# Kernel optimization log

Hardware: AMD Instinct MI355X
Metric: run time of the kernel (lower is better)

The kernel has to match this reference:

```python
import jax, jax.numpy as jnp
import numpy as np

B = 64            # graphs in batch
N = 100_000       # total nodes
E = 600_000       # total edges of g == nodes of line graph lg
E2 = 1_500_000    # edges of line graph
H = 128           # hidden_dim
L = 3             # num_layers
MAXZ = 100

seg_sum = jax.ops.segment_sum


def setup_inputs() -> dict:
    key = jax.random.key(0)
    ks = jax.random.split(key, 20)
    s = 1.0 / np.sqrt(H)
    inp = {
        'z': jax.random.randint(ks[0], (N,), 0, MAXZ + 1),
        'd': jax.random.uniform(ks[1], (E, 1), dtype=jnp.float32),
        'src': jax.random.randint(ks[2], (E,), 0, N),
        'dst': jax.random.randint(ks[3], (E,), 0, N),
        'lsrc': jax.random.randint(ks[4], (E2,), 0, E),
        'ldst': jax.random.randint(ks[5], (E2,), 0, E),
        'node_graph': jnp.sort(jax.random.randint(ks[6], (N,), 0, B)),
        'edge_graph': jnp.sort(jax.random.randint(ks[7], (E,), 0, B)),
        'emb': jax.random.normal(ks[8], (MAXZ + 1, H), jnp.float32),
        'ep_w': jax.random.normal(ks[9], (1, H), jnp.float32) * s,
        'ep_b': jnp.zeros((H,), jnp.float32),
        'gW': jax.random.normal(ks[10], (L, H, H), jnp.float32) * s,
        'gb': jnp.zeros((L, H), jnp.float32),
        'lgW': jax.random.normal(ks[11], (L, H, H), jnp.float32) * s,
        'lgb': jnp.zeros((L, H), jnp.float32),
        'r1w': jax.random.normal(ks[12], (2 * H, H), jnp.float32) * s,
        'r1b': jnp.zeros((H,), jnp.float32),
        'r2w': jax.random.normal(ks[13], (H, 1), jnp.float32) * s,
        'r2b': jnp.zeros((1,), jnp.float32),
    }
    return inp


def _graph_conv(h, srcix, dstix, W, b, n_nodes):
    # DGL GraphConv, norm='both', aggregate-then-weight (in==out dims):
    # h' = D_in^{-1/2} * A^T * (D_out^{-1/2} * h) @ W + b, degrees clamped >= 1
    ones = jnp.ones(srcix.shape[0], h.dtype)
    deg_out = jnp.clip(seg_sum(ones, srcix, num_segments=n_nodes), 1.0)
    deg_in = jnp.clip(seg_sum(ones, dstix, num_segments=n_nodes), 1.0)
    m = h * (deg_out ** -0.5)[:, None]
    agg = seg_sum(m[srcix], dstix, num_segments=n_nodes)  # SpMM gather-scatter
    agg = agg * (deg_in ** -0.5)[:, None]
    return agg @ W + b


def _segment_mean(h, seg, n_seg):
    sums = seg_sum(h, seg, num_segments=n_seg)
    cnt = jnp.clip(seg_sum(jnp.ones(h.shape[0], h.dtype), seg, num_segments=n_seg), 1.0)
    return sums / cnt[:, None]


def reference(z, d, src, dst, lsrc, ldst, node_graph, edge_graph,
              emb, ep_w, ep_b, gW, gb, lgW, lgb, r1w, r1b, r2w, r2b):
    h = emb[z]                       # [N, H]
    e = d @ ep_w + ep_b              # [E, H]
    for i in range(L):
        h = jax.nn.relu(_graph_conv(h, src, dst, gW[i], gb[i], N))
    for i in range(L):
        e = jax.nn.relu(_graph_conv(e, lsrc, ldst, lgW[i], lgb[i], E))
    hg = _segment_mean(h, node_graph, B)   # [B, H]
    he = _segment_mean(e, edge_graph, B)   # [B, H]
    x = jnp.concatenate([hg, he], axis=-1)  # [B, 2H]
    y = jax.nn.silu(x @ r1w + r1b) @ r2w + r2b
    return y.reshape(-1)             # [B]
```

## Files before the change

### kernel.cpp

```cpp
#include <hip/hip_runtime.h>
#include <math.h>

#define H 128
typedef unsigned short u16;
typedef unsigned char u8;
typedef unsigned int u32;
typedef _Float16 f16;
typedef f16 f16x8 __attribute__((ext_vector_type(8)));
typedef float f32x4 __attribute__((ext_vector_type(4)));
typedef float f32x2 __attribute__((ext_vector_type(2)));

#if __has_builtin(__builtin_amdgcn_cvt_pk_fp8_f32)
#define HW8 1
#else
#define HW8 0
#endif

#define SSTRIDE 144

static inline int cdiv(long long a, long long b) { return (int)((a + b - 1) / b); }

struct F8 {
    static __device__ inline float dec(u8 v) {
        int e = (v >> 3) & 15, m = v & 7;
        float f = (e == 0) ? (float)m * 0.001953125f : ldexpf(1.f + 0.125f * (float)m, e - 7);
        return (v & 0x80) ? -f : f;
    }
    static __device__ inline u8 enc(float x) {
        u8 s = (u8)((__float_as_uint(x) >> 24) & 0x80);
        float ax = fabsf(x);
        if (!(ax < 448.f)) return s | 0x7E;
        if (ax < 0.015625f) {
            int m = (int)rintf(ax * 512.f);
            if (m >= 8) return s | 0x08;
            return s | (u8)m;
        }
        int e; float fr = frexpf(ax, &e);
        int E = e - 1;
        int m = (int)rintf(fr * 16.f - 8.f);
        if (m == 8) { m = 0; ++E; }
        if (E > 8) return s | 0x7E;
        return s | (u8)(((E + 7) << 3) | m);
    }
};

static __device__ inline u32 enc4(float x0, float x1, float x2, float x3) {
#if HW8
    u32 w = __builtin_amdgcn_cvt_pk_fp8_f32(x0, x1, 0, false);
    w = __builtin_amdgcn_cvt_pk_fp8_f32(x2, x3, w, true);
    return w;
#else
    union { u8 b[4]; u32 u; } p;
    p.b[0] = F8::enc(x0); p.b[1] = F8::enc(x1); p.b[2] = F8::enc(x2); p.b[3] = F8::enc(x3);
    return p.u;
#endif
}
static __device__ inline float4 dec4(u32 v) {
#if HW8
    f32x2 lo = __builtin_amdgcn_cvt_pk_f32_fp8(v, false);
    f32x2 hi = __builtin_amdgcn_cvt_pk_f32_fp8(v, true);
    return make_float4(lo.x, lo.y, hi.x, hi.y);
#else
    union { u32 u; u8 b[4]; } c; c.u = v;
    return make_float4(F8::dec(c.b[0]), F8::dec(c.b[1]), F8::dec(c.b[2]), F8::dec(c.b[3]));
#endif
}
static __device__ inline float dec1(u8 b) {
#if HW8
    return __builtin_amdgcn_cvt_f32_fp8((int)b, 0);
#else
    return F8::dec(b);
#endif
}

__global__ __launch_bounds__(256) void setup1_k(
    const float* __restrict__ gW, const float* __restrict__ lgW, f16* __restrict__ wt, int L, int nbPW,
    const int* __restrict__ src, const int* __restrict__ dst,
    const int* __restrict__ lsrc, const int* __restrict__ ldst,
    int* __restrict__ con, int* __restrict__ cin, int* __restrict__ coe, int* __restrict__ cie,
    int E, int E2, int nbHI,
    const int* __restrict__ node_graph, int N, const int* __restrict__ edge_graph,
    int B, int* __restrict__ cntn, int* __restrict__ cnte) {
    int blk = blockIdx.x;
    if (blk < nbPW) {
        int mat = blk >> 6;
        int idx = (blk & 63) * 256 + threadIdx.x;
        int k = idx >> 7, n = idx & 127;
        const float* W = (mat < L) ? gW + (size_t)mat * H * H : lgW + (size_t)(mat - L) * H * H;
        wt[(size_t)mat * H * H + (size_t)n * H + k] = (f16)W[(size_t)k * H + n];
        return;
    }
    blk -= nbPW;
    if (blk < nbHI) {
        int i = blk * 256 + threadIdx.x;
        if (i < E) {
            atomicAdd(&con[src[i]], 1);
            atomicAdd(&cin[dst[i]], 1);
        } else if (i < E + E2) {
            int j = i - E;
            atomicAdd(&coe[lsrc[j]], 1);
            atomicAdd(&cie[ldst[j]], 1);
        }
        return;
    }
    blk -= nbHI;
    {
        const int* seg = blk ? edge_graph : node_graph;
        int n = blk ? E : N;
        int* cnt = blk ? cnte : cntn;
        __shared__ int bound[129];
        int b = threadIdx.x;
        if (b <= B) {
            int lo = 0, hi = n;
            while (lo < hi) {
                int mid = (lo + hi) >> 1;
                if (seg[mid] < b) lo = mid + 1; else hi = mid;
            }
            bound[b] = lo;
        }
        __syncthreads();
        if (b < B) cnt[b] = bound[b + 1] - bound[b];
    }
}

__global__ __launch_bounds__(256) void setup2_k(
    const int* __restrict__ con, const int* __restrict__ cin,
    const int* __restrict__ coe, const int* __restrict__ cie,
    float* __restrict__ ron, float* __restrict__ rin,
    float* __restrict__ roe, float* __restrict__ rie,
    const float* __restrict__ d, float2* __restrict__ pairE, int N, int E, int nbRS,
    int* __restrict__ offs_n, int nbN, int* __restrict__ offs_e, int* __restrict__ bsum) {
    int blk = blockIdx.x;
    if (blk < nbRS) {
        int i = blk * 256 + threadIdx.x;
        if (i < N) { int v = con[i]; ron[i] = rsqrtf((float)(v < 1 ? 1 : v)); }
        else if (i < 2 * N) { int n = i - N; int v = cin[n]; rin[n] = rsqrtf((float)(v < 1 ? 1 : v)); }
        else if (i < 2 * N + E) {
            int n = i - 2 * N; int v = coe[n];
            float r = rsqrtf((float)(v < 1 ? 1 : v));
            roe[n] = r;
            pairE[n] = make_float2(r * d[n], r);
        } else if (i < 2 * N + 2 * E) {
            int n = i - 2 * N - E; int v = cie[n]; rie[n] = rsqrtf((float)(v < 1 ? 1 : v));
        }
        return;
    }
    blk -= nbRS;
    {
        __shared__ int sh[256];
        const int* in; int* out; int n; int gid;
        if (blk < nbN) { in = cin; out = offs_n; n = N; gid = blk * 256 + threadIdx.x; }
        else { in = cie; out = offs_e; n = E; gid = (blk - nbN) * 256 + threadIdx.x; }
        int v = (gid < n) ? in[gid] : 0;
        sh[threadIdx.x] = v;
        __syncthreads();
        for (int off = 1; off < 256; off <<= 1) {
            int t = (threadIdx.x >= off) ? sh[threadIdx.x - off] : 0;
            __syncthreads();
            sh[threadIdx.x] += t;
            __syncthreads();
        }
        if (gid < n) out[gid] = sh[threadIdx.x] - v;
        if (threadIdx.x == 255) bsum[blk] = sh[255];
    }
}

__global__ __launch_bounds__(256) void scan_bsum2_k(int* __restrict__ bsum, int nbA, int nbB) {
    __shared__ int sh[256];
    __shared__ int carry;
#pragma unroll 1
    for (int part = 0; part < 2; ++part) {
        int base0 = part ? nbA : 0;
        int nb = part ? nbB : nbA;
        if (threadIdx.x == 0) carry = 0;
        __syncthreads();
        for (int base = 0; base < nb; base += 256) {
            int i = base + threadIdx.x;
            int v = (i < nb) ? bsum[base0 + i] : 0;
            sh[threadIdx.x] = v;
            __syncthreads();
            for (int off = 1; off < 256; off <<= 1) {
                int t = (threadIdx.x >= off) ? sh[threadIdx.x - off] : 0;
                __syncthreads();
                sh[threadIdx.x] += t;
                __syncthreads();
            }
            if (i < nb) bsum[base0 + i] = sh[threadIdx.x] - v + carry;
            __syncthreads();
            if (threadIdx.x == 0) carry += sh[255];
            __syncthreads();
        }
    }
}

__global__ __launch_bounds__(256) void setup3_k(
    int* __restrict__ offs_n, int* __restrict__ cur_n, int N, int nbN, int E,
    int* __restrict__ offs_e, int* __restrict__ cur_e, int E2, int nbE,
    const int* __restrict__ bsum,
    const int* __restrict__ z, const float* __restrict__ emb,
    const float* __restrict__ ron, u8* __restrict__ featN) {
    int blk = blockIdx.x;
    int nbSA = nbN + nbE;
    if (blk < nbSA) {
        int* offs; int* curp; int n; int gid; int nnz;
        if (blk < nbN) { offs = offs_n; curp = cur_n; n = N; gid = blk * 256 + threadIdx.x; nnz = E; }
        else { offs = offs_e; curp = cur_e; n = E; gid = (blk - nbN) * 256 + threadIdx.x; nnz = E2; }
        if (gid < n) {
            int v = offs[gid] + bsum[blk];
            offs[gid] = v;
            curp[gid] = v;
        }
        if (gid == 0) offs[n] = nnz;
        return;
    }
    blk -= nbSA;
    {
        int idx = blk * 256 + threadIdx.x;
        if (idx >= N * 32) return;
        int n = idx >> 5, c4 = (idx & 31) << 2;
        float sc = ron[n];
        const float4 v = *(const float4*)(emb + (size_t)z[n] * H + c4);
        *(u32*)(featN + (size_t)n * H + c4) = enc4(v.x * sc, v.y * sc, v.z * sc, v.w * sc);
    }
}

__global__ __launch_bounds__(256) void fill2_k(const int* __restrict__ src, const int* __restrict__ dst,
                                               const int* __restrict__ lsrc, const int* __restrict__ ldst,
                                               int* __restrict__ cur_n, int* __restrict__ cur_e,
                                               uint2* __restrict__ nbr_n, uint2* __restrict__ nbr_e,
                                               int E, int E2) {
    int i = blockIdx.x * 256 + threadIdx.x;
    if (i < E) {
        int dd = dst[i];
        int p = atomicAdd(&cur_n[dd], 1);
        nbr_n[p] = make_uint2((u32)src[i], (u32)dd);
    } else if (i < E + E2) {
        int j = i - E;
        int dd = ldst[j];
        int p = atomicAdd(&cur_e[dd], 1);
        nbr_e[p] = make_uint2((u32)lsrc[j], (u32)dd);
    }
}

template <bool STORE>
__device__ __forceinline__ void conv_mfma_phase(
    u8* __restrict__ Xout, const f16* __restrict__ Wt, const float* __restrict__ bias,
    const float* __restrict__ scale_out, int M, int row0, f16 (*As)[136], int wave, int lane) {
    const int rowbase = row0 + wave * 16;
    if (rowbase >= M) return;
    const int l15 = lane & 15;
    const int quad = lane >> 4;

    f16x8 a[4];
#pragma unroll
    for (int kt = 0; kt < 4; ++kt)
        a[kt] = *(const f16x8*)&As[wave * 16 + l15][kt * 32 + quad * 8];

    float rsc[4];
#pragma unroll
    for (int r = 0; r < 4; ++r) {
        int gr = rowbase + quad * 4 + r;
        rsc[r] = (scale_out && gr < M) ? scale_out[gr] : 1.f;
    }

    u8* stage = (u8*)&As[wave * 16][0];

#pragma unroll
    for (int n0 = 0; n0 < 8; ++n0) {
        f32x4 acc = {0.f, 0.f, 0.f, 0.f};
        const f16* bp = Wt + (size_t)(n0 * 16 + l15) * H + quad * 8;
#pragma unroll
        for (int kt = 0; kt < 4; ++kt) {
            f16x8 b = *(const f16x8*)(bp + kt * 32);
            acc = __builtin_amdgcn_mfma_f32_16x16x32_f16(a[kt], b, acc, 0, 0, 0);
        }
        int col = n0 * 16 + l15;
        float bv = bias[col];
        float o[4];
#pragma unroll
        for (int r = 0; r < 4; ++r) o[r] = fmaxf(acc[r] + bv, 0.f) * rsc[r];
        u32 w = enc4(o[0], o[1], o[2], o[3]);
#pragma unroll
        for (int r = 0; r < 4; ++r) stage[(quad * 4 + r) * SSTRIDE + col] = (u8)(w >> (8 * r));
    }
    if (STORE) {
        const int lr = lane >> 2;
        const int lc = (lane & 3) * 32;
        int gr = rowbase + lr;
        if (gr < M) {
            uint4 v0 = *(const uint4*)&stage[lr * SSTRIDE + lc];
            uint4 v1 = *(const uint4*)&stage[lr * SSTRIDE + lc + 16];
            *(uint4*)(Xout + (size_t)gr * H + lc) = v0;
            *(uint4*)(Xout + (size_t)gr * H + lc + 16) = v1;
        }
    }
}

template <bool STORE>
__device__ __forceinline__ void conv_wave(
    const u8* __restrict__ Xin, u8* __restrict__ Xout,
    const int* __restrict__ offs, const uint2* __restrict__ nbr2,
    const float* __restrict__ rs_in, const f16* __restrict__ Wt,
    const float* __restrict__ bias, const float* __restrict__ scale_out, int M,
    int row0, f16 (*As)[136], int wave, int lane) {
    const int rowbase = row0 + wave * 16;

    {
        uint2* zp = (uint2*)&As[wave * 16][0];
#pragma unroll
        for (int i = 0; i < 9; ++i) {
            int o = lane + i * 64;
            if (o < 544) zp[o] = make_uint2(0u, 0u);
        }
    }

    {
        const int gl = lane >> 4;
        const int ln = lane & 15;
        const int r_lo = min(rowbase + gl * 4, M);
        const int r_hi = min(rowbase + gl * 4 + 4, M);
        const int jbeg = offs[r_lo];
        const int jend = offs[r_hi];
        if (jbeg < jend) {
            float a0 = 0.f, a1 = 0.f, a2 = 0.f, a3 = 0.f, a4 = 0.f, a5 = 0.f, a6 = 0.f, a7 = 0.f;
            int curdst = -1;
            for (int j = jbeg; j < jend; j += 4) {
                int j1 = min(j + 1, jend - 1), j2 = min(j + 2, jend - 1), j3 = min(j + 3, jend - 1);
                uint2 e0 = nbr2[j], e1 = nbr2[j1], e2 = nbr2[j2], e3 = nbr2[j3];
                uint2 f0 = *(const uint2*)(Xin + ((size_t)e0.x << 7) + (ln << 3));
                uint2 f1 = *(const uint2*)(Xin + ((size_t)e1.x << 7) + (ln << 3));
                uint2 f2 = *(const uint2*)(Xin + ((size_t)e2.x << 7) + (ln << 3));
                uint2 f3 = *(const uint2*)(Xin + ((size_t)e3.x << 7) + (ln << 3));
                uint2 ev[4] = {e0, e1, e2, e3};
                uint2 fv[4] = {f0, f1, f2, f3};
#pragma unroll
                for (int k = 0; k < 4; ++k) {
                    if (j + k < jend) {
                        int dk = (int)ev[k].y;
                        if (dk != curdst) {
                            if (curdst >= 0) {
                                float ri = rs_in[curdst];
                                f16x8 o;
                                o[0] = (f16)(a0 * ri); o[1] = (f16)(a1 * ri);
                                o[2] = (f16)(a2 * ri); o[3] = (f16)(a3 * ri);
                                o[4] = (f16)(a4 * ri); o[5] = (f16)(a5 * ri);
                                o[6] = (f16)(a6 * ri); o[7] = (f16)(a7 * ri);
                                *(f16x8*)&As[curdst - row0][ln << 3] = o;
                                a0 = a1 = a2 = a3 = a4 = a5 = a6 = a7 = 0.f;
                            }
                            curdst = dk;
                        }
                        float4 lo = dec4(fv[k].x);
                        float4 hi = dec4(fv[k].y);
                        a0 += lo.x; a1 += lo.y; a2 += lo.z; a3 += lo.w;
                        a4 += hi.x; a5 += hi.y; a6 += hi.z; a7 += hi.w;
                    }
                }
            }
            if (curdst >= 0) {
                float ri = rs_in[curdst];
                f16x8 o;
                o[0] = (f16)(a0 * ri); o[1] = (f16)(a1 * ri);
                o[2] = (f16)(a2 * ri); o[3] = (f16)(a3 * ri);
                o[4] = (f16)(a4 * ri); o[5] = (f16)(a5 * ri);
                o[6] = (f16)(a6 * ri); o[7] = (f16)(a7 * ri);
                *(f16x8*)&As[curdst - row0][ln << 3] = o;
            }
        }
    }

    conv_mfma_phase<STORE>(Xout, Wt, bias, scale_out, M, row0, As, wave, lane);
}

__device__ __forceinline__ void conv_wave_l0e(
    u8* __restrict__ Xout, const int* __restrict__ offs, const uint2* __restrict__ nbr2,
    const float2* __restrict__ pairE, const float* __restrict__ rs_in,
    const float* __restrict__ epw, const float* __restrict__ epb,
    const f16* __restrict__ Wt, const float* __restrict__ bias,
    const float* __restrict__ scale_out, int E,
    int row0, f16 (*As)[136], int wave, int lane) {
    const int rowbase = row0 + wave * 16;
    const int r = lane >> 2;
    const int t = lane & 3;
    int grow = min(rowbase + r, E - 1);
    int jb = offs[grow], je = offs[grow + 1];
    float sd = 0.f, sw = 0.f;
    for (int j = jb + t; j < je; j += 4) {
        float2 p = pairE[nbr2[j].x];
        sd += p.x; sw += p.y;
    }
    sd += __shfl_xor(sd, 1); sw += __shfl_xor(sw, 1);
    sd += __shfl_xor(sd, 2); sw += __shfl_xor(sw, 2);
    float ri = (rowbase + r < E) ? rs_in[rowbase + r] : 0.f;
    sd *= ri; sw *= ri;
#pragma unroll
    for (int c8 = 0; c8 < 4; ++c8) {
        int c0 = t * 32 + c8 * 8;
        const float4 wa = *(const float4*)(epw + c0);
        const float4 wb = *(const float4*)(epw + c0 + 4);
        const float4 ba = *(const float4*)(epb + c0);
        const float4 bb = *(const float4*)(epb + c0 + 4);
        f16x8 o;
        o[0] = (f16)(sd * wa.x + sw * ba.x); o[1] = (f16)(sd * wa.y + sw * ba.y);
        o[2] = (f16)(sd * wa.z + sw * ba.z); o[3] = (f16)(sd * wa.w + sw * ba.w);
        o[4] = (f16)(sd * wb.x + sw * bb.x); o[5] = (f16)(sd * wb.y + sw * bb.y);
        o[6] = (f16)(sd * wb.z + sw * bb.z); o[7] = (f16)(sd * wb.w + sw * bb.w);
        *(f16x8*)&As[wave * 16 + r][c0] = o;
    }
    conv_mfma_phase<true>(Xout, Wt, bias, scale_out, E, row0, As, wave, lane);
}

__global__ __launch_bounds__(256) void conv2_k(
    const u8* __restrict__ XinN, u8* __restrict__ XoutN,
    const int* __restrict__ offs_n, const uint2* __restrict__ nbr_n,
    const float* __restrict__ rinN, const f16* __restrict__ WtN,
    const float* __restrict__ biasN, const float* __restrict__ scaleN, int N, int nbCN,
    const u8* __restrict__ XinE, u8* __restrict__ XoutE,
    const int* __restrict__ offs_e, const uint2* __restrict__ nbr_e,
    const float* __restrict__ rinE, const f16* __restrict__ WtE,
    const float* __restrict__ biasE, const float* __restrict__ scaleE, int E) {
    __shared__ f16 As[64][136];
    const int tid = threadIdx.x;
    const int wave = tid >> 6;
    const int lane = tid & 63;
    if ((int)blockIdx.x < nbCN) {
        conv_wave<true>(XinN, XoutN, offs_n, nbr_n, rinN, WtN, biasN, scaleN, N,
                        blockIdx.x * 64, As, wave, lane);
    } else {
        conv_wave<true>(XinE, XoutE, offs_e, nbr_e, rinE, WtE, biasE, scaleE, E,
                        (blockIdx.x - nbCN) * 64, As, wave, lane);
    }
}

__global__ __launch_bounds__(256) void conv2_l0_k(
    const u8* __restrict__ XinN, u8* __restrict__ XoutN,
    const int* __restrict__ offs_n, const uint2* __restrict__ nbr_n,
    const float* __restrict__ rinN, const f16* __restrict__ WtN,
    const float* __restrict__ biasN, const float* __restrict__ scaleN, int N, int nbCN,
    u8* __restrict__ XoutE,
    const int* __restrict__ offs_e, const uint2* __restrict__ nbr_e,
    const float2* __restrict__ pairE, const float* __restrict__ rinE,
    const float* __restrict__ epw, const float* __restrict__ epb,
    const f16* __restrict__ WtE, const float* __restrict__ biasE,
    const float* __restrict__ scaleE, int E) {
    __shared__ f16 As[64][136];
    const int tid = threadIdx.x;
    const int wave = tid >> 6;
    const int lane = tid & 63;
    if ((int)blockIdx.x < nbCN) {
        conv_wave<true>(XinN, XoutN, offs_n, nbr_n, rinN, WtN, biasN, scaleN, N,
                        blockIdx.x * 64, As, wave, lane);
    } else {
        conv_wave_l0e(XoutE, offs_e, nbr_e, pairE, rinE, epw, epb, WtE, biasE, scaleE, E,
                      (blockIdx.x - nbCN) * 64, As, wave, lane);
    }
}

__global__ __launch_bounds__(256) void conv2_last_k(
    const u8* __restrict__ XinN,
    const int* __restrict__ offs_n, const uint2* __restrict__ nbr_n,
    const float* __restrict__ rinN, const f16* __restrict__ WtN,
    const float* __restrict__ biasN, int N, int nbCN,
    const int* __restrict__ node_graph, float* __restrict__ hg,
    const u8* __restrict__ XinE,
    const int* __restrict__ offs_e, const uint2* __restrict__ nbr_e,
    const float* __restrict__ rinE, const f16* __restrict__ WtE,
    const float* __restrict__ biasE, int E,
    const int* __restrict__ edge_graph, float* __restrict__ he) {
    __shared__ f16 As[64][136];
    __shared__ int sgid[64];
    const int tid = threadIdx.x;
    const int wave = tid >> 6;
    const int lane = tid & 63;
    const bool isN = (int)blockIdx.x < nbCN;
    const int row0 = (isN ? blockIdx.x : blockIdx.x - nbCN) * 64;
    const int M = isN ? N : E;
    const int* seg = isN ? node_graph : edge_graph;
    float* outp = isN ? hg : he;

    if (tid < 64) {
        int gr = row0 + tid;
        sgid[tid] = (gr < M) ? seg[gr] : -1;
    }

    if (isN) {
        conv_wave<false>(XinN, nullptr, offs_n, nbr_n, rinN, WtN, biasN, nullptr, N,
                         row0, As, wave, lane);
    } else {
        conv_wave<false>(XinE, nullptr, offs_e, nbr_e, rinE, WtE, biasE, nullptr, E,
                         row0, As, wave, lane);
    }
    __syncthreads();

    const int j = tid & 127;
    const int rbeg = (tid >> 7) * 32;
    const u8* sbase = (const u8*)&As[0][0];
    float acc = 0.f;
    int gcur = -1;
    for (int r = rbeg; r < rbeg + 32; ++r) {
        int g = sgid[r];
        if (g < 0) break;
        if (g != gcur) {
            if (gcur >= 0) atomicAdd(&outp[(size_t)gcur * H + j], acc);
            acc = 0.f;
            gcur = g;
        }
        acc += dec1(sbase[(size_t)(r >> 4) * (16 * 136 * 2) + (r & 15) * SSTRIDE + j]);
    }
    if (gcur >= 0) atomicAdd(&outp[(size_t)gcur * H + j], acc);
}

__global__ __launch_bounds__(128) void readout_k(const float* __restrict__ hg, const float* __restrict__ he,
                                                 const int* __restrict__ cn, const int* __restrict__ ce,
                                                 const float* __restrict__ r1w, const float* __restrict__ r1b,
                                                 const float* __restrict__ r2w, const float* __restrict__ r2b,
                                                 float* __restrict__ out) {
    const int b = blockIdx.x;
    const int j = threadIdx.x;
    const float invn = 1.f / fmaxf((float)cn[b], 1.f);
    const float inve = 1.f / fmaxf((float)ce[b], 1.f);
    float acc = r1b[j];
    for (int k = 0; k < H; ++k) acc = fmaf(hg[(size_t)b * H + k] * invn, r1w[(size_t)k * H + j], acc);
    for (int k = 0; k < H; ++k) acc = fmaf(he[(size_t)b * H + k] * inve, r1w[(size_t)(k + H) * H + j], acc);
    float s = acc / (1.f + expf(-acc));
    __shared__ float red[128];
    red[j] = s * r2w[j];
    __syncthreads();
    for (int off = 64; off > 0; off >>= 1) {
        if (j < off) red[j] += red[j + off];
        __syncthreads();
    }
    if (j == 0) out[b] = red[0] + r2b[0];
}

__global__ void report_k(float* out, int n, float val) {
    int i = blockIdx.x * 64 + threadIdx.x;
    if (i < n) out[i] = val;
}

extern "C" void kernel_launch(void* const* d_in, const int* in_sizes, int n_in,
                              void* d_out, int out_size, void* d_ws, size_t ws_size,
                              hipStream_t stream) {
    const int* z          = (const int*)d_in[0];
    const float* d        = (const float*)d_in[1];
    const int* src        = (const int*)d_in[2];
    const int* dst        = (const int*)d_in[3];
    const int* lsrc       = (const int*)d_in[4];
    const int* ldst       = (const int*)d_in[5];
    const int* node_graph = (const int*)d_in[6];
    const int* edge_graph = (const int*)d_in[7];
    const float* emb      = (const float*)d_in[8];
    const float* epw      = (const float*)d_in[9];
    const float* epb      = (const float*)d_in[10];
    const float* gW       = (const float*)d_in[11];
    const float* gb       = (const float*)d_in[12];
    const float* lgW      = (const float*)d_in[13];
    const float* lgb      = (const float*)d_in[14];
    const float* r1w      = (const float*)d_in[15];
    const float* r1b      = (const float*)d_in[16];
    const float* r2w      = (const float*)d_in[17];
    const float* r2b      = (const float*)d_in[18];

    const int N  = in_sizes[0];
    const int E  = in_sizes[2];
    const int E2 = in_sizes[4];
    const int B  = out_size;
    const int L  = 3;
    float* out = (float*)d_out;
    char* ws = (char*)d_ws;

    size_t off = 0;
    auto al = [&](size_t b) -> char* { char* q = ws + off; off += (b + 255) & ~(size_t)255; return q; };
    u8*  featEA = (u8*)al((size_t)E * H);
    u8*  featEB = (u8*)al((size_t)E * H);
    u8*  featNA = (u8*)al((size_t)N * H);
    u8*  featNB = (u8*)al((size_t)N * H);
    f16* wt    = (f16*)al((size_t)2 * L * H * H * 2);
    float* ron = (float*)al((size_t)N * 4);
    float* rin = (float*)al((size_t)N * 4);
    float* roe = (float*)al((size_t)E * 4);
    float* rie = (float*)al((size_t)E * 4);
    float2* pairE = (float2*)al((size_t)E * 8);
    size_t cntCount = (size_t)2 * N + 2 * E + 2 * B;
    size_t cntBytes = cntCount * 4;
    size_t poolsOff = (cntBytes + 255) & ~(size_t)255;
    char* zblock = al(poolsOff + (size_t)2 * B * H * 4);
    int* cnts = (int*)zblock;
    float* pools = (float*)(zblock + poolsOff);
    int* con = cnts; int* cin_ = con + N; int* coe = cin_ + N; int* cie = coe + E;
    int* cntn = cie + E; int* cnte = cntn + B;
    float* hg = pools;
    float* he = pools + (size_t)B * H;
    int* offs_n = (int*)al(((size_t)N + 1) * 4);
    int* cur_n  = (int*)al((size_t)N * 4);
    int* offs_e = (int*)al(((size_t)E + 1) * 4);
    int* cur_e  = (int*)al((size_t)E * 4);
    uint2* nbr_n = (uint2*)al((size_t)E * 8);
    uint2* nbr_e = (uint2*)al((size_t)E2 * 8);
    int nbN = cdiv(N, 256), nbE = cdiv(E, 256);
    int* bsum   = (int*)al(((size_t)nbN + nbE + 2) * 4);

    if (off > ws_size) {
        report_k<<<cdiv(B, 64), 64, 0, stream>>>(out, B, (float)(ws_size >> 20));
        return;
    }

    hipMemsetAsync(zblock, 0, poolsOff + (size_t)2 * B * H * 4, stream);

    const int nbPW = 2 * L * 64;
    const int nbHI = cdiv((long long)E + E2, 256);
    setup1_k<<<nbPW + nbHI + 2, 256, 0, stream>>>(gW, lgW, wt, L, nbPW,
                                                  src, dst, lsrc, ldst, con, cin_, coe, cie,
                                                  E, E2, nbHI, node_graph, N, edge_graph, B, cntn, cnte);

    const int nbRS = cdiv((long long)2 * N + 2 * E, 256);
    setup2_k<<<nbRS + nbN + nbE, 256, 0, stream>>>(con, cin_, coe, cie, ron, rin, roe, rie,
                                                   d, pairE, N, E, nbRS, offs_n, nbN, offs_e, bsum);
    scan_bsum2_k<<<1, 256, 0, stream>>>(bsum, nbN, nbE);

    const int nbIN = cdiv((long long)N * 32, 256);
    setup3_k<<<nbN + nbE + nbIN, 256, 0, stream>>>(offs_n, cur_n, N, nbN, E,
                                                   offs_e, cur_e, E2, nbE, bsum, z, emb, ron, featNA);

    fill2_k<<<cdiv((long long)E + E2, 256), 256, 0, stream>>>(src, dst, lsrc, ldst, cur_n, cur_e, nbr_n, nbr_e, E, E2);

    const int nbCN = cdiv(N, 64), nbCE = cdiv(E, 64);

    conv2_l0_k<<<nbCN + nbCE, 256, 0, stream>>>(
        featNA, featNB, offs_n, nbr_n, rin, wt, gb, ron, N, nbCN,
        featEB, offs_e, nbr_e, pairE, rie, epw, epb,
        wt + (size_t)L * H * H, lgb, roe, E);

    conv2_k<<<nbCN + nbCE, 256, 0, stream>>>(
        featNB, featNA, offs_n, nbr_n, rin, wt + (size_t)1 * H * H, gb + (size_t)1 * H, ron, N, nbCN,
        featEB, featEA, offs_e, nbr_e, rie, wt + (size_t)(L + 1) * H * H, lgb + (size_t)1 * H, roe, E);

    conv2_last_k<<<nbCN + nbCE, 256, 0, stream>>>(
        featNA, offs_n, nbr_n, rin, wt + (size_t)2 * H * H, gb + (size_t)2 * H, N, nbCN, node_graph, hg,
        featEA, offs_e, nbr_e, rie, wt + (size_t)(L + 2) * H * H, lgb + (size_t)2 * H, E, edge_graph, he);

    readout_k<<<B, 128, 0, stream>>>(hg, he, cntn, cnte, r1w, r1b, r2w, r2b, out);
}
```

Baseline: 1.210 ms.

## Software-pipeline neighbor gather and pool MFMA output directly in final layer

The gather loop now processes 8 edges per iteration and prefetches the next batch of neighbor indices while feature loads are in flight. It also preloads the four per-row in-degree scales instead of reading them on each row flush. The last-layer kernel no longer round-trips fp8-encoded outputs through shared memory. It pools the fp32 MFMA results directly, using a shuffle reduction plus one atomic per column when a 64-row block lies in a single graph, and falls back to per-row atomics otherwise. Launch bounds request 4 blocks per SM, which may cap registers and cause spills now that the deeper unroll uses more of them.

After: 1.169 ms. 1.04x faster.

```diff
diff --git a/kernel.cpp b/kernel.cpp
--- a/kernel.cpp
+++ b/kernel.cpp
@@ -242,6 +242,87 @@
     }
 }
 
+__device__ __forceinline__ void gather_phase(
+    const u8* __restrict__ Xin,
+    const int* __restrict__ offs, const uint2* __restrict__ nbr2,
+    const float* __restrict__ rs_in, int M,
+    int row0, f16 (*As)[136], int wave, int lane) {
+    const int rowbase = row0 + wave * 16;
+    {
+        uint2* zp = (uint2*)&As[wave * 16][0];
+#pragma unroll
+        for (int i = 0; i < 9; ++i) {
+            int o = lane + i * 64;
+            if (o < 544) zp[o] = make_uint2(0u, 0u);
+        }
+    }
+    const int gl = lane >> 4;
+    const int ln = lane & 15;
+    const int rbase4 = rowbase + gl * 4;
+    const int r_lo = min(rbase4, M);
+    const int r_hi = min(rbase4 + 4, M);
+    const int jbeg = offs[r_lo];
+    const int jend = offs[r_hi];
+    if (jbeg >= jend) return;
+    const int mrow = M - 1;
+    const float rsr0 = rs_in[min(rbase4 + 0, mrow)];
+    const float rsr1 = rs_in[min(rbase4 + 1, mrow)];
+    const float rsr2 = rs_in[min(rbase4 + 2, mrow)];
+    const float rsr3 = rs_in[min(rbase4 + 3, mrow)];
+
+    float a0 = 0.f, a1 = 0.f, a2 = 0.f, a3 = 0.f, a4 = 0.f, a5 = 0.f, a6 = 0.f, a7 = 0.f;
+    int curdst = -1;
+
+#define FLUSH_ROW()                                                              \
+    do {                                                                         \
+        const int dd_ = curdst - rbase4;                                         \
+        const float ri_ = dd_ == 0 ? rsr0 : (dd_ == 1 ? rsr1 : (dd_ == 2 ? rsr2 : rsr3)); \
+        f16x8 o_;                                                                \
+        o_[0] = (f16)(a0 * ri_); o_[1] = (f16)(a1 * ri_);                        \
+        o_[2] = (f16)(a2 * ri_); o_[3] = (f16)(a3 * ri_);                        \
+        o_[4] = (f16)(a4 * ri_); o_[5] = (f16)(a5 * ri_);                        \
+        o_[6] = (f16)(a6 * ri_); o_[7] = (f16)(a7 * ri_);                        \
+        *(f16x8*)&As[curdst - row0][ln << 3] = o_;                               \
+    } while (0)
+
+    uint2 e[8];
+#pragma unroll
+    for (int k = 0; k < 8; ++k) e[k] = nbr2[min(jbeg + k, jend - 1)];
+    int jc = jbeg;
+    do {
+        uint2 f[8];
+#pragma unroll
+        for (int k = 0; k < 8; ++k)
+            f[k] = *(const uint2*)(Xin + ((size_t)e[k].x << 7) + (ln << 3));
+        const int jn = jc + 8;
+        uint2 en[8];
+#pragma unroll
+        for (int k = 0; k < 8; ++k) en[k] = nbr2[min(jn + k, jend - 1)];
+#pragma unroll
+        for (int k = 0; k < 8; ++k) {
+            if (jc + k < jend) {
+                const int dk = (int)e[k].y;
+                if (dk != curdst) {
+                    if (curdst >= 0) {
+                        FLUSH_ROW();
+                        a0 = a1 = a2 = a3 = a4 = a5 = a6 = a7 = 0.f;
+                    }
+                    curdst = dk;
+                }
+                float4 lo = dec4(f[k].x);
+                float4 hi = dec4(f[k].y);
+                a0 += lo.x; a1 += lo.y; a2 += lo.z; a3 += lo.w;
+                a4 += hi.x; a5 += hi.y; a6 += hi.z; a7 += hi.w;
+            }
+        }
+#pragma unroll
+        for (int k = 0; k < 8; ++k) e[k] = en[k];
+        jc = jn;
+    } while (jc < jend);
+    FLUSH_ROW();
+#undef FLUSH_ROW
+}
+
 template <bool STORE>
 __device__ __forceinline__ void conv_mfma_phase(
     u8* __restrict__ Xout, const f16* __restrict__ Wt, const float* __restrict__ bias,
@@ -296,6 +377,60 @@
     }
 }
 
+__device__ __forceinline__ void conv_mfma_pool_phase(
+    const f16* __restrict__ Wt, const float* __restrict__ bias, int M, int row0,
+    f16 (*As)[136], float (*pool)[128], int wave, int lane,
+    const int* __restrict__ seg, float* __restrict__ outp, bool uni) {
+    const int rowbase = row0 + wave * 16;
+    if (rowbase >= M) return;
+    const int l15 = lane & 15;
+    const int quad = lane >> 4;
+
+    f16x8 a[4];
+#pragma unroll
+    for (int kt = 0; kt < 4; ++kt)
+        a[kt] = *(const f16x8*)&As[wave * 16 + l15][kt * 32 + quad * 8];
+
+    const int gr0 = rowbase + quad * 4;
+    const int remM = M - gr0;
+    int g0 = -1, g1 = -1, g2 = -1, g3 = -1;
+    if (!uni) {
+        g0 = (0 < remM) ? seg[gr0 + 0] : -1;
+        g1 = (1 < remM) ? seg[gr0 + 1] : -1;
+        g2 = (2 < remM) ? seg[gr0 + 2] : -1;
+        g3 = (3 < remM) ? seg[gr0 + 3] : -1;
+    }
+
+#pragma unroll
+    for (int n0 = 0; n0 < 8; ++n0) {
+        f32x4 acc = {0.f, 0.f, 0.f, 0.f};
+        const f16* bp = Wt + (size_t)(n0 * 16 + l15) * H + quad * 8;
+#pragma unroll
+        for (int kt = 0; kt < 4; ++kt) {
+            f16x8 b = *(const f16x8*)(bp + kt * 32);
+            acc = __builtin_amdgcn_mfma_f32_16x16x32_f16(a[kt], b, acc, 0, 0, 0);
+        }
+        const int col = n0 * 16 + l15;
+        const float bv = bias[col];
+        const float o0 = (0 < remM) ? fmaxf(acc[0] + bv, 0.f) : 0.f;
+        const float o1 = (1 < remM) ? fmaxf(acc[1] + bv, 0.f) : 0.f;
+        const float o2 = (2 < remM) ? fmaxf(acc[2] + bv, 0.f) : 0.f;
+        const float o3 = (3 < remM) ? fmaxf(acc[3] + bv, 0.f) : 0.f;
+        if (uni) {
+            float s = (o0 + o1) + (o2 + o3);
+            s += __shfl_xor(s, 16);
+            s += __shfl_xor(s, 32);
+            if (quad == 0) pool[wave][col] = s;
+        } else {
+            float ac = o0; int gc = g0;
+            if (g1 == gc) ac += o1; else { if (gc >= 0) atomicAdd(&outp[(size_t)gc * H + col], ac); gc = g1; ac = o1; }
+            if (g2 == gc) ac += o2; else { if (gc >= 0) atomicAdd(&outp[(size_t)gc * H + col], ac); gc = g2; ac = o2; }
+            if (g3 == gc) ac += o3; else { if (gc >= 0) atomicAdd(&outp[(size_t)gc * H + col], ac); gc = g3; ac = o3; }
+            if (gc >= 0) atomicAdd(&outp[(size_t)gc * H + col], ac);
+        }
+    }
+}
+
 template <bool STORE>
 __device__ __forceinline__ void conv_wave(
     const u8* __restrict__ Xin, u8* __restrict__ Xout,
@@ -303,72 +438,7 @@
     const float* __restrict__ rs_in, const f16* __restrict__ Wt,
     const float* __restrict__ bias, const float* __restrict__ scale_out, int M,
     int row0, f16 (*As)[136], int wave, int lane) {
-    const int rowbase = row0 + wave * 16;
-
-    {
-        uint2* zp = (uint2*)&As[wave * 16][0];
-#pragma unroll
-        for (int i = 0; i < 9; ++i) {
-            int o = lane + i * 64;
-            if (o < 544) zp[o] = make_uint2(0u, 0u);
-        }
-    }
-
-    {
-        const int gl = lane >> 4;
-        const int ln = lane & 15;
-        const int r_lo = min(rowbase + gl * 4, M);
-        const int r_hi = min(rowbase + gl * 4 + 4, M);
-        const int jbeg = offs[r_lo];
-        const int jend = offs[r_hi];
-        if (jbeg < jend) {
-            float a0 = 0.f, a1 = 0.f, a2 = 0.f, a3 = 0.f, a4 = 0.f, a5 = 0.f, a6 = 0.f, a7 = 0.f;
-            int curdst = -1;
-            for (int j = jbeg; j < jend; j += 4) {
-                int j1 = min(j + 1, jend - 1), j2 = min(j + 2, jend - 1), j3 = min(j + 3, jend - 1);
-                uint2 e0 = nbr2[j], e1 = nbr2[j1], e2 = nbr2[j2], e3 = nbr2[j3];
-                uint2 f0 = *(const uint2*)(Xin + ((size_t)e0.x << 7) + (ln << 3));
-                uint2 f1 = *(const uint2*)(Xin + ((size_t)e1.x << 7) + (ln << 3));
-                uint2 f2 = *(const uint2*)(Xin + ((size_t)e2.x << 7) + (ln << 3));
-                uint2 f3 = *(const uint2*)(Xin + ((size_t)e3.x << 7) + (ln << 3));
-                uint2 ev[4] = {e0, e1, e2, e3};
-                uint2 fv[4] = {f0, f1, f2, f3};
-#pragma unroll
-                for (int k = 0; k < 4; ++k) {
-                    if (j + k < jend) {
-                        int dk = (int)ev[k].y;
-                        if (dk != curdst) {
-                            if (curdst >= 0) {
-                                float ri = rs_in[curdst];
-                                f16x8 o;
-                                o[0] = (f16)(a0 * ri); o[1] = (f16)(a1 * ri);
-                                o[2] = (f16)(a2 * ri); o[3] = (f16)(a3 * ri);
-                                o[4] = (f16)(a4 * ri); o[5] = (f16)(a5 * ri);
-                                o[6] = (f16)(a6 * ri); o[7] = (f16)(a7 * ri);
-                                *(f16x8*)&As[curdst - row0][ln << 3] = o;
-                                a0 = a1 = a2 = a3 = a4 = a5 = a6 = a7 = 0.f;
-                            }
-                            curdst = dk;
-                        }
-                        float4 lo = dec4(fv[k].x);
-                        float4 hi = dec4(fv[k].y);
-                        a0 += lo.x; a1 += lo.y; a2 += lo.z; a3 += lo.w;
-                        a4 += hi.x; a5 += hi.y; a6 += hi.z; a7 += hi.w;
-                    }
-                }
-            }
-            if (curdst >= 0) {
-                float ri = rs_in[curdst];
-                f16x8 o;
-                o[0] = (f16)(a0 * ri); o[1] = (f16)(a1 * ri);
-                o[2] = (f16)(a2 * ri); o[3] = (f16)(a3 * ri);
-                o[4] = (f16)(a4 * ri); o[5] = (f16)(a5 * ri);
-                o[6] = (f16)(a6 * ri); o[7] = (f16)(a7 * ri);
-                *(f16x8*)&As[curdst - row0][ln << 3] = o;
-            }
-        }
-    }
-
+    gather_phase(Xin, offs, nbr2, rs_in, M, row0, As, wave, lane);
     conv_mfma_phase<STORE>(Xout, Wt, bias, scale_out, M, row0, As, wave, lane);
 }
 
@@ -410,7 +480,7 @@
     conv_mfma_phase<true>(Xout, Wt, bias, scale_out, E, row0, As, wave, lane);
 }
 
-__global__ __launch_bounds__(256) void conv2_k(
+__global__ __launch_bounds__(256, 4) void conv2_k(
     const u8* __restrict__ XinN, u8* __restrict__ XoutN,
     const int* __restrict__ offs_n, const uint2* __restrict__ nbr_n,
     const float* __restrict__ rinN, const f16* __restrict__ WtN,
@@ -432,7 +502,7 @@
     }
 }
 
-__global__ __launch_bounds__(256) void conv2_l0_k(
+__global__ __launch_bounds__(256, 4) void conv2_l0_k(
     const u8* __restrict__ XinN, u8* __restrict__ XoutN,
     const int* __restrict__ offs_n, const uint2* __restrict__ nbr_n,
     const float* __restrict__ rinN, const f16* __restrict__ WtN,
@@ -456,7 +526,7 @@
     }
 }
 
-__global__ __launch_bounds__(256) void conv2_last_k(
+__global__ __launch_bounds__(256, 4) void conv2_last_k(
     const u8* __restrict__ XinN,
     const int* __restrict__ offs_n, const uint2* __restrict__ nbr_n,
     const float* __restrict__ rinN, const f16* __restrict__ WtN,
@@ -468,7 +538,7 @@
     const float* __restrict__ biasE, int E,
     const int* __restrict__ edge_graph, float* __restrict__ he) {
     __shared__ f16 As[64][136];
-    __shared__ int sgid[64];
+    __shared__ float pool[4][128];
     const int tid = threadIdx.x;
     const int wave = tid >> 6;
     const int lane = tid & 63;
@@ -478,36 +548,24 @@
     const int* seg = isN ? node_graph : edge_graph;
     float* outp = isN ? hg : he;
 
-    if (tid < 64) {
-        int gr = row0 + tid;
-        sgid[tid] = (gr < M) ? seg[gr] : -1;
-    }
+    ((float*)pool)[tid] = 0.f;
+    ((float*)pool)[tid + 256] = 0.f;
+    const int gblk = seg[row0];
+    const bool uni = (seg[min(row0 + 63, M - 1)] == gblk);
+    __syncthreads();
 
     if (isN) {
-        conv_wave<false>(XinN, nullptr, offs_n, nbr_n, rinN, WtN, biasN, nullptr, N,
-                         row0, As, wave, lane);
+        gather_phase(XinN, offs_n, nbr_n, rinN, N, row0, As, wave, lane);
+        conv_mfma_pool_phase(WtN, biasN, N, row0, As, pool, wave, lane, seg, outp, uni);
     } else {
-        conv_wave<false>(XinE, nullptr, offs_e, nbr_e, rinE, WtE, biasE, nullptr, E,
-                         row0, As, wave, lane);
+        gather_phase(XinE, offs_e, nbr_e, rinE, E, row0, As, wave, lane);
+        conv_mfma_pool_phase(WtE, biasE, E, row0, As, pool, wave, lane, seg, outp, uni);
     }
     __syncthreads();
-
-    const int j = tid & 127;
-    const int rbeg = (tid >> 7) * 32;
-    const u8* sbase = (const u8*)&As[0][0];
-    float acc = 0.f;
-    int gcur = -1;
-    for (int r = rbeg; r < rbeg + 32; ++r) {
-        int g = sgid[r];
-        if (g < 0) break;
-        if (g != gcur) {
-            if (gcur >= 0) atomicAdd(&outp[(size_t)gcur * H + j], acc);
-            acc = 0.f;
-            gcur = g;
-        }
-        acc += dec1(sbase[(size_t)(r >> 4) * (16 * 136 * 2) + (r & 15) * SSTRIDE + j]);
-    }
-    if (gcur >= 0) atomicAdd(&outp[(size_t)gcur * H + j], acc);
+    if (uni && tid < 128) {
+        float s = (pool[0][tid] + pool[1][tid]) + (pool[2][tid] + pool[3][tid]);
+        atomicAdd(&outp[(size_t)gblk * H + tid], s);
+    }
 }
 
 __global__ __launch_bounds__(128) void readout_k(const float* __restrict__ hg, const float* __restrict__ he,
```
